# Kernel tuning notes

Hardware: AMD Instinct MI355X
Metric: run time of the kernel (lower is better)

Reference implementation:

```python
import jax, jax.numpy as jnp
import numpy as np

NUM_CLASSES = 100000   # vocab (input_dim of the layer)
DIM = 256              # embedding dim (output_dim of the layer)
BATCH = 256
NUM_TRUE = 1024        # hardcoded num_true in call()
NUM_SAMPLED = 16384    # hardcoded num_sampled in call()
LOG_RANGE = float(np.log(NUM_CLASSES + 1.0))


def _sample_log_uniform_unique(rng, n, range_max):
    # Mimics tf log_uniform_candidate_sampler with unique=True: rejection-sample
    # from P(c) ~ log((c+2)/(c+1)) until n unique ids are collected.
    seen = {}
    log_range = np.log(range_max + 1.0)
    while len(seen) < n:
        u = rng.uniform(0.0, log_range, size=2 * n)
        ids = np.minimum(np.floor(np.exp(u) - 1.0).astype(np.int64), range_max - 1)
        for v in ids.tolist():
            if len(seen) >= n:
                break
            seen[v] = None
    return np.fromiter(seen.keys(), dtype=np.int64, count=n)


def setup_inputs() -> dict:
    key = jax.random.key(0)
    k1, k2, k3, k4 = jax.random.split(key, 4)
    inputs = jax.random.normal(k1, (BATCH, DIM), jnp.float32)
    # Original inits w/b to zeros; use small random values for a non-degenerate baseline.
    w = jax.random.normal(k2, (NUM_CLASSES, DIM), jnp.float32) * 0.02
    b = jax.random.normal(k3, (NUM_CLASSES,), jnp.float32) * 0.02
    labels = jax.random.randint(k4, (BATCH, NUM_TRUE), 0, NUM_CLASSES, dtype=jnp.int32)
    rng = np.random.default_rng(0)
    sampled = jnp.asarray(_sample_log_uniform_unique(rng, NUM_SAMPLED, NUM_CLASSES), jnp.int32)
    return {"inputs": inputs, "w": w, "b": b, "labels": labels, "sampled": sampled}


def _log_uniform_prob(ids):
    idf = ids.astype(jnp.float32)
    return jnp.log((idf + 2.0) / (idf + 1.0)) / LOG_RANGE


def _expected_count(ids):
    # P(id appears among NUM_SAMPLED unique candidates) = 1 - (1-p)^NUM_SAMPLED
    p = _log_uniform_prob(ids)
    return -jnp.expm1(NUM_SAMPLED * jnp.log1p(-p))


def _sigmoid_xent(logits, target):
    # numerically stable sigmoid cross-entropy, target is a scalar label value
    return jnp.maximum(logits, 0.0) - logits * target + jnp.log1p(jnp.exp(-jnp.abs(logits)))


def reference(inputs, w, b, labels, sampled):
    # true logits: per-example dot with each true class row  [B, T]
    true_w = w[labels]                                    # [B, T, D] gather
    true_logits = jnp.einsum('bd,btd->bt', inputs, true_w) + b[labels]
    true_logits = true_logits - jnp.log(_expected_count(labels))
    # sampled logits: shared candidate set  [B, S]
    sampled_logits = inputs @ w[sampled].T + b[sampled]
    sampled_logits = sampled_logits - jnp.log(_expected_count(sampled))
    # NCE targets: 1/num_true for true classes, 0 for sampled; sum over columns
    true_xent = _sigmoid_xent(true_logits, 1.0 / NUM_TRUE)
    sampled_xent = _sigmoid_xent(sampled_logits, 0.0)
    return true_xent.sum(axis=1) + sampled_xent.sum(axis=1)   # [B]
```

## Files before the change

kernel.cpp:

```cpp
#include <hip/hip_runtime.h>
#include <hip/hip_bf16.h>

#define NUM_CLASSES 100000
#define DIM 256
#define BATCH 256
#define NUM_TRUE 1024
#define NUM_SAMPLED 16384
#define LOG_RANGE 11.51293546492023f
#define INV_LOG_RANGE (1.0f / LOG_RANGE)

typedef __bf16 bf16x8 __attribute__((ext_vector_type(8)));
typedef float  f32x4  __attribute__((ext_vector_type(4)));

static __device__ __forceinline__ unsigned short f2bf(float f) {
    unsigned int u = __float_as_uint(f);
    unsigned int lsb = (u >> 16) & 1u;
    u += 0x7fffu + lsb;
    return (unsigned short)(u >> 16);
}

static __device__ __forceinline__ float neg_log_ec(int id) {
    float idf = (float)id;
    float p = logf((idf + 2.0f) / (idf + 1.0f)) * INV_LOG_RANGE;
    float ec = -expm1f((float)NUM_SAMPLED * log1pf(-p));
    return -logf(ec);
}

static __device__ __forceinline__ void fma4(float4& acc, float4 a, float4 b) {
    acc.x = fmaf(a.x, b.x, acc.x);
    acc.y = fmaf(a.y, b.y, acc.y);
    acc.z = fmaf(a.z, b.z, acc.z);
    acc.w = fmaf(a.w, b.w, acc.w);
}

__global__ __launch_bounds__(256) void conv_inputs(const float* __restrict__ in,
                                                   unsigned short* __restrict__ out) {
    int idx = blockIdx.x * 256 + threadIdx.x;
    float4 v = ((const float4*)in)[idx];
    ushort4 p;
    p.x = f2bf(v.x); p.y = f2bf(v.y); p.z = f2bf(v.z); p.w = f2bf(v.w);
    ((ushort4*)out)[idx] = p;
}

__global__ __launch_bounds__(256) void true_kernel(const float* __restrict__ inputs,
                                                   const float* __restrict__ w,
                                                   const float* __restrict__ bias,
                                                   const int* __restrict__ labels,
                                                   float* __restrict__ out) {
    __shared__ __align__(16) float ins[DIM];
    __shared__ float wsum[4];
    const int tid = threadIdx.x;
    const int b = blockIdx.y;
    ins[tid] = inputs[b * DIM + tid];
    __syncthreads();

    const int t = blockIdx.x * 256 + tid;
    const int l = labels[b * NUM_TRUE + t];
    const float bl = bias[l];
    const float4* __restrict__ wr = (const float4*)(w + (size_t)l * DIM);
    const float4* __restrict__ ir = (const float4*)ins;

    float4 a0 = {0,0,0,0}, a1 = {0,0,0,0}, a2 = {0,0,0,0}, a3 = {0,0,0,0};
    #pragma unroll 4
    for (int k = 0; k < 16; ++k) {
        float4 w0 = wr[k * 4 + 0];
        float4 w1 = wr[k * 4 + 1];
        float4 w2 = wr[k * 4 + 2];
        float4 w3 = wr[k * 4 + 3];
        fma4(a0, w0, ir[k * 4 + 0]);
        fma4(a1, w1, ir[k * 4 + 1]);
        fma4(a2, w2, ir[k * 4 + 2]);
        fma4(a3, w3, ir[k * 4 + 3]);
    }
    float dot = (a0.x + a0.y + a0.z + a0.w) + (a1.x + a1.y + a1.z + a1.w)
              + (a2.x + a2.y + a2.z + a2.w) + (a3.x + a3.y + a3.z + a3.w);

    float logit = dot + bl + neg_log_ec(l);
    const float tgt = 1.0f / (float)NUM_TRUE;
    float v = fmaxf(logit, 0.0f) - logit * tgt + log1pf(expf(-fabsf(logit)));

    v += __shfl_xor(v, 1);  v += __shfl_xor(v, 2);  v += __shfl_xor(v, 4);
    v += __shfl_xor(v, 8);  v += __shfl_xor(v, 16); v += __shfl_xor(v, 32);
    if ((tid & 63) == 0) wsum[tid >> 6] = v;
    __syncthreads();
    if (tid == 0) atomicAdd(&out[b], wsum[0] + wsum[1] + wsum[2] + wsum[3]);
}

#define LWS 264
__global__ __launch_bounds__(256) void sampled_kernel(const float* __restrict__ w,
                                                      const float* __restrict__ bias,
                                                      const int* __restrict__ sampled,
                                                      const unsigned short* __restrict__ inbf,
                                                      float* __restrict__ partial) {
    __shared__ unsigned short lw[64][LWS];
    __shared__ unsigned short li[64][LWS];
    __shared__ float cs[64];
    __shared__ float bacc[BATCH];

    const int tid = threadIdx.x;
    const int s0 = blockIdx.x * 64;
    bacc[tid] = 0.0f;

    const int row = tid & 63;
    const int seg = tid >> 6;
    {
        const int id = sampled[s0 + row];
        const float4* src = (const float4*)(w + (size_t)id * DIM + seg * 64);
        #pragma unroll
        for (int j = 0; j < 16; ++j) {
            float4 v = src[j];
            ushort4 pk;
            pk.x = f2bf(v.x); pk.y = f2bf(v.y); pk.z = f2bf(v.z); pk.w = f2bf(v.w);
            *(ushort4*)(&lw[row][seg * 64 + j * 4]) = pk;
        }
        if (seg == 0) cs[row] = bias[id] + neg_log_ec(id);
    }

    const int lane = tid & 63;
    const int wv   = tid >> 6;
    const int m    = lane & 15;
    const int quad = lane >> 4;
    const int wy   = wv & 1;
    const int wx   = wv >> 1;

    for (int chunk = 0; chunk < 4; ++chunk) {
        __syncthreads();
        {
            const int4* isrc = (const int4*)(inbf + ((chunk * 64 + row) * DIM + seg * 64));
            int4* idst = (int4*)(&li[row][seg * 64]);
            #pragma unroll
            for (int j = 0; j < 8; ++j) idst[j] = isrc[j];
        }
        __syncthreads();

        f32x4 acc00 = {0,0,0,0}, acc01 = {0,0,0,0}, acc10 = {0,0,0,0}, acc11 = {0,0,0,0};
        const unsigned short* pa0 = &lw[wy * 32 + m][quad * 8];
        const unsigned short* pa1 = &lw[wy * 32 + 16 + m][quad * 8];
        const unsigned short* pb0 = &li[wx * 32 + m][quad * 8];
        const unsigned short* pb1 = &li[wx * 32 + 16 + m][quad * 8];
        #pragma unroll
        for (int kk = 0; kk < 8; ++kk) {
            bf16x8 a0 = *(const bf16x8*)(pa0 + kk * 32);
            bf16x8 a1 = *(const bf16x8*)(pa1 + kk * 32);
            bf16x8 b0 = *(const bf16x8*)(pb0 + kk * 32);
            bf16x8 b1 = *(const bf16x8*)(pb1 + kk * 32);
            acc00 = __builtin_amdgcn_mfma_f32_16x16x32_bf16(a0, b0, acc00, 0, 0, 0);
            acc01 = __builtin_amdgcn_mfma_f32_16x16x32_bf16(a0, b1, acc01, 0, 0, 0);
            acc10 = __builtin_amdgcn_mfma_f32_16x16x32_bf16(a1, b0, acc10, 0, 0, 0);
            acc11 = __builtin_amdgcn_mfma_f32_16x16x32_bf16(a1, b1, acc11, 0, 0, 0);
        }

        float ps0 = 0.0f, ps1 = 0.0f;
        #pragma unroll
        for (int r = 0; r < 4; ++r) {
            {
                float c = cs[wy * 32 + quad * 4 + r];
                float l0 = acc00[r] + c;
                ps0 += fmaxf(l0, 0.0f) + __logf(1.0f + __expf(-fabsf(l0)));
                float l1 = acc01[r] + c;
                ps1 += fmaxf(l1, 0.0f) + __logf(1.0f + __expf(-fabsf(l1)));
            }
            {
                float c = cs[wy * 32 + 16 + quad * 4 + r];
                float l0 = acc10[r] + c;
                ps0 += fmaxf(l0, 0.0f) + __logf(1.0f + __expf(-fabsf(l0)));
                float l1 = acc11[r] + c;
                ps1 += fmaxf(l1, 0.0f) + __logf(1.0f + __expf(-fabsf(l1)));
            }
        }
        ps0 += __shfl_xor(ps0, 16); ps0 += __shfl_xor(ps0, 32);
        ps1 += __shfl_xor(ps1, 16); ps1 += __shfl_xor(ps1, 32);
        if (quad == 0) {
            atomicAdd(&bacc[chunk * 64 + wx * 32 + m], ps0);
            atomicAdd(&bacc[chunk * 64 + wx * 32 + 16 + m], ps1);
        }
    }
    __syncthreads();
    partial[blockIdx.x * BATCH + tid] = bacc[tid];
}

__global__ __launch_bounds__(256) void reduce_kernel(const float* __restrict__ partial,
                                                     float* __restrict__ out) {
    __shared__ float wsum[4];
    const int b = blockIdx.x;
    const int tid = threadIdx.x;
    float v = partial[tid * BATCH + b];
    v += __shfl_xor(v, 1);  v += __shfl_xor(v, 2);  v += __shfl_xor(v, 4);
    v += __shfl_xor(v, 8);  v += __shfl_xor(v, 16); v += __shfl_xor(v, 32);
    if ((tid & 63) == 0) wsum[tid >> 6] = v;
    __syncthreads();
    if (tid == 0) out[b] += wsum[0] + wsum[1] + wsum[2] + wsum[3];
}

extern "C" void kernel_launch(void* const* d_in, const int* in_sizes, int n_in,
                              void* d_out, int out_size, void* d_ws, size_t ws_size,
                              hipStream_t stream) {
    const float* inputs  = (const float*)d_in[0];
    const float* w       = (const float*)d_in[1];
    const float* bias    = (const float*)d_in[2];
    const int*   labels  = (const int*)d_in[3];
    const int*   sampled = (const int*)d_in[4];
    float* out = (float*)d_out;

    unsigned short* inbf = (unsigned short*)d_ws;
    float* partial = (float*)((char*)d_ws + BATCH * DIM * 2);

    hipMemsetAsync(out, 0, BATCH * sizeof(float), stream);
    conv_inputs<<<64, 256, 0, stream>>>(inputs, inbf);
    true_kernel<<<dim3(4, 256), 256, 0, stream>>>(inputs, w, bias, labels, out);
    sampled_kernel<<<NUM_SAMPLED / 64, 256, 0, stream>>>(w, bias, sampled, inbf, partial);
    reduce_kernel<<<BATCH, 256, 0, stream>>>(partial, out);
}
```

Baseline: 209.0 us.

## Coalesce true-class gathers, precompute per-class bias term, split sampled batch

The true-logit kernel now has 16 lanes share each label row, so every gathered weight row is read with coalesced float4 loads, and the next row is prefetched while the current dot product runs. A new per-class kernel precomputes bias plus the negative log expected count once for all classes, which removes the transcendental work from both logit kernels. The standalone input-to-bf16 conversion is folded into the sampled kernel. The sampled kernel's grid is split over two batch halves to double its parallelism, at the cost of gathering and converting each sampled weight tile twice and computing the comb term for all 100k classes.

Measured after the change: 195.1 us. 1.07x faster.

```diff
diff --git a/kernel.cpp b/kernel.cpp
--- a/kernel.cpp
+++ b/kernel.cpp
@@ -26,25 +26,19 @@
     return -logf(ec);
 }
 
-static __device__ __forceinline__ void fma4(float4& acc, float4 a, float4 b) {
-    acc.x = fmaf(a.x, b.x, acc.x);
-    acc.y = fmaf(a.y, b.y, acc.y);
-    acc.z = fmaf(a.z, b.z, acc.z);
-    acc.w = fmaf(a.w, b.w, acc.w);
-}
-
-__global__ __launch_bounds__(256) void conv_inputs(const float* __restrict__ in,
-                                                   unsigned short* __restrict__ out) {
-    int idx = blockIdx.x * 256 + threadIdx.x;
-    float4 v = ((const float4*)in)[idx];
-    ushort4 p;
-    p.x = f2bf(v.x); p.y = f2bf(v.y); p.z = f2bf(v.z); p.w = f2bf(v.w);
-    ((ushort4*)out)[idx] = p;
+static __device__ __forceinline__ float dot4(float4 a, float4 b) {
+    return fmaf(a.x, b.x, fmaf(a.y, b.y, fmaf(a.z, b.z, a.w * b.w)));
+}
+
+__global__ __launch_bounds__(256) void comb_kernel(const float* __restrict__ bias,
+                                                   float* __restrict__ comb) {
+    int c = blockIdx.x * 256 + threadIdx.x;
+    if (c < NUM_CLASSES) comb[c] = bias[c] + neg_log_ec(c);
 }
 
 __global__ __launch_bounds__(256) void true_kernel(const float* __restrict__ inputs,
                                                    const float* __restrict__ w,
-                                                   const float* __restrict__ bias,
+                                                   const float* __restrict__ comb,
                                                    const int* __restrict__ labels,
                                                    float* __restrict__ out) {
     __shared__ __align__(16) float ins[DIM];
@@ -54,52 +48,65 @@
     ins[tid] = inputs[b * DIM + tid];
     __syncthreads();
 
-    const int t = blockIdx.x * 256 + tid;
-    const int l = labels[b * NUM_TRUE + t];
-    const float bl = bias[l];
-    const float4* __restrict__ wr = (const float4*)(w + (size_t)l * DIM);
-    const float4* __restrict__ ir = (const float4*)ins;
-
-    float4 a0 = {0,0,0,0}, a1 = {0,0,0,0}, a2 = {0,0,0,0}, a3 = {0,0,0,0};
-    #pragma unroll 4
-    for (int k = 0; k < 16; ++k) {
-        float4 w0 = wr[k * 4 + 0];
-        float4 w1 = wr[k * 4 + 1];
-        float4 w2 = wr[k * 4 + 2];
-        float4 w3 = wr[k * 4 + 3];
-        fma4(a0, w0, ir[k * 4 + 0]);
-        fma4(a1, w1, ir[k * 4 + 1]);
-        fma4(a2, w2, ir[k * 4 + 2]);
-        fma4(a3, w3, ir[k * 4 + 3]);
-    }
-    float dot = (a0.x + a0.y + a0.z + a0.w) + (a1.x + a1.y + a1.z + a1.w)
-              + (a2.x + a2.y + a2.z + a2.w) + (a3.x + a3.y + a3.z + a3.w);
-
-    float logit = dot + bl + neg_log_ec(l);
-    const float tgt = 1.0f / (float)NUM_TRUE;
-    float v = fmaxf(logit, 0.0f) - logit * tgt + log1pf(expf(-fabsf(logit)));
-
-    v += __shfl_xor(v, 1);  v += __shfl_xor(v, 2);  v += __shfl_xor(v, 4);
-    v += __shfl_xor(v, 8);  v += __shfl_xor(v, 16); v += __shfl_xor(v, 32);
-    if ((tid & 63) == 0) wsum[tid >> 6] = v;
+    const int lane = tid & 63;
+    const int wv   = tid >> 6;
+    const int sub  = lane >> 4;
+    const int part = lane & 15;
+    const float4* ir = (const float4*)ins;
+    const float4 in0 = ir[part], in1 = ir[16 + part], in2 = ir[32 + part], in3 = ir[48 + part];
+
+    const int* lab = labels + b * NUM_TRUE + blockIdx.x * 128 + wv * 32;
+
+    float acc = 0.0f;
+    float4 w0, w1, w2, w3;
+    float cl;
+    {
+        int l = lab[sub];
+        const float4* wr = (const float4*)(w + (size_t)l * DIM);
+        w0 = wr[part]; w1 = wr[16 + part]; w2 = wr[32 + part]; w3 = wr[48 + part];
+        cl = comb[l];
+    }
+
+    #pragma unroll
+    for (int i = 0; i < 8; ++i) {
+        float4 n0 = {0,0,0,0}, n1 = {0,0,0,0}, n2 = {0,0,0,0}, n3 = {0,0,0,0};
+        float cn = 0.0f;
+        if (i < 7) {
+            int ln = lab[(i + 1) * 4 + sub];
+            const float4* wr = (const float4*)(w + (size_t)ln * DIM);
+            n0 = wr[part]; n1 = wr[16 + part]; n2 = wr[32 + part]; n3 = wr[48 + part];
+            cn = comb[ln];
+        }
+        float d = dot4(w0, in0) + dot4(w1, in1) + dot4(w2, in2) + dot4(w3, in3);
+        d += __shfl_xor(d, 1); d += __shfl_xor(d, 2);
+        d += __shfl_xor(d, 4); d += __shfl_xor(d, 8);
+        float logit = d + cl;
+        float v = fmaxf(logit, 0.0f) - logit * (1.0f / (float)NUM_TRUE)
+                + log1pf(expf(-fabsf(logit)));
+        acc += (part == 0) ? v : 0.0f;
+        w0 = n0; w1 = n1; w2 = n2; w3 = n3; cl = cn;
+    }
+    acc += __shfl_xor(acc, 16); acc += __shfl_xor(acc, 32);
+    if (lane == 0) wsum[wv] = acc;
     __syncthreads();
     if (tid == 0) atomicAdd(&out[b], wsum[0] + wsum[1] + wsum[2] + wsum[3]);
 }
 
 #define LWS 264
 __global__ __launch_bounds__(256) void sampled_kernel(const float* __restrict__ w,
-                                                      const float* __restrict__ bias,
+                                                      const float* __restrict__ comb,
                                                       const int* __restrict__ sampled,
-                                                      const unsigned short* __restrict__ inbf,
+                                                      const float* __restrict__ inputs,
                                                       float* __restrict__ partial) {
     __shared__ unsigned short lw[64][LWS];
     __shared__ unsigned short li[64][LWS];
     __shared__ float cs[64];
-    __shared__ float bacc[BATCH];
+    __shared__ float bacc[128];
 
     const int tid = threadIdx.x;
     const int s0 = blockIdx.x * 64;
-    bacc[tid] = 0.0f;
+    const int bhalf = blockIdx.y;
+    if (tid < 128) bacc[tid] = 0.0f;
 
     const int row = tid & 63;
     const int seg = tid >> 6;
@@ -113,7 +120,7 @@
             pk.x = f2bf(v.x); pk.y = f2bf(v.y); pk.z = f2bf(v.z); pk.w = f2bf(v.w);
             *(ushort4*)(&lw[row][seg * 64 + j * 4]) = pk;
         }
-        if (seg == 0) cs[row] = bias[id] + neg_log_ec(id);
+        if (seg == 0) cs[row] = comb[id];
     }
 
     const int lane = tid & 63;
@@ -123,13 +130,18 @@
     const int wy   = wv & 1;
     const int wx   = wv >> 1;
 
-    for (int chunk = 0; chunk < 4; ++chunk) {
+    for (int chunk = 0; chunk < 2; ++chunk) {
         __syncthreads();
         {
-            const int4* isrc = (const int4*)(inbf + ((chunk * 64 + row) * DIM + seg * 64));
-            int4* idst = (int4*)(&li[row][seg * 64]);
+            const int bg = bhalf * 128 + chunk * 64 + row;
+            const float4* isrc = (const float4*)(inputs + bg * DIM + seg * 64);
             #pragma unroll
-            for (int j = 0; j < 8; ++j) idst[j] = isrc[j];
+            for (int j = 0; j < 16; ++j) {
+                float4 v = isrc[j];
+                ushort4 pk;
+                pk.x = f2bf(v.x); pk.y = f2bf(v.y); pk.z = f2bf(v.z); pk.w = f2bf(v.w);
+                *(ushort4*)(&li[row][seg * 64 + j * 4]) = pk;
+            }
         }
         __syncthreads();
 
@@ -176,7 +188,8 @@
         }
     }
     __syncthreads();
-    partial[blockIdx.x * BATCH + tid] = bacc[tid];
+    if (tid < 128)
+        partial[(bhalf * 256 + blockIdx.x) * 128 + tid] = bacc[tid];
 }
 
 __global__ __launch_bounds__(256) void reduce_kernel(const float* __restrict__ partial,
@@ -184,7 +197,8 @@
     __shared__ float wsum[4];
     const int b = blockIdx.x;
     const int tid = threadIdx.x;
-    float v = partial[tid * BATCH + b];
+    const int y = b >> 7, lb = b & 127;
+    float v = partial[(y * 256 + tid) * 128 + lb];
     v += __shfl_xor(v, 1);  v += __shfl_xor(v, 2);  v += __shfl_xor(v, 4);
     v += __shfl_xor(v, 8);  v += __shfl_xor(v, 16); v += __shfl_xor(v, 32);
     if ((tid & 63) == 0) wsum[tid >> 6] = v;
@@ -202,12 +216,12 @@
     const int*   sampled = (const int*)d_in[4];
     float* out = (float*)d_out;
 
-    unsigned short* inbf = (unsigned short*)d_ws;
-    float* partial = (float*)((char*)d_ws + BATCH * DIM * 2);
+    float* comb    = (float*)d_ws;
+    float* partial = (float*)((char*)d_ws + 409600);
 
     hipMemsetAsync(out, 0, BATCH * sizeof(float), stream);
-    conv_inputs<<<64, 256, 0, stream>>>(inputs, inbf);
-    true_kernel<<<dim3(4, 256), 256, 0, stream>>>(inputs, w, bias, labels, out);
-    sampled_kernel<<<NUM_SAMPLED / 64, 256, 0, stream>>>(w, bias, sampled, inbf, partial);
+    comb_kernel<<<(NUM_CLASSES + 255) / 256, 256, 0, stream>>>(bias, comb);
+    true_kernel<<<dim3(8, 256), 256, 0, stream>>>(inputs, w, comb, labels, out);
+    sampled_kernel<<<dim3(256, 2), 256, 0, stream>>>(w, comb, sampled, inputs, partial);
     reduce_kernel<<<BATCH, 256, 0, stream>>>(partial, out);
 }
```
